# Kernel optimization log

Measured on AMD Instinct MI355X. Metric: run time of the kernel, lower is better.

Reference implementation:

```python
import jax, jax.numpy as jnp
import numpy as np
import math

D_TOKEN = 1024
N_HEADS = 16
D_HEADS = D_TOKEN // N_HEADS
B, S = 8, 4096


def setup_inputs() -> dict:
    key = jax.random.key(0)
    ks = jax.random.split(key, 8)
    scale = 1.0 / math.sqrt(D_TOKEN)
    inp = {
        "x_q": jax.random.normal(ks[0], (B, S, D_TOKEN), dtype=jnp.float32),
        "x_kv": jax.random.normal(ks[1], (B, S, D_TOKEN), dtype=jnp.float32),
        # Linear weights stored torch-style [out, in]
        "q_w": jax.random.normal(ks[2], (D_TOKEN, D_TOKEN), dtype=jnp.float32) * scale,
        "k_w": jax.random.normal(ks[3], (D_TOKEN, D_TOKEN), dtype=jnp.float32) * scale,
        "v_w": jax.random.normal(ks[4], (D_TOKEN, D_TOKEN), dtype=jnp.float32) * scale,
        "wq_w": jax.random.normal(ks[5], (N_HEADS, D_TOKEN), dtype=jnp.float32) * scale,
        "wk_w": jax.random.normal(ks[6], (N_HEADS, D_TOKEN), dtype=jnp.float32) * scale,
        "out_w": jax.random.normal(ks[7], (D_TOKEN, D_TOKEN), dtype=jnp.float32) * scale,
        # biases zero-initialized in the original module
        "q_b": jnp.zeros((D_TOKEN,), jnp.float32),
        "k_b": jnp.zeros((D_TOKEN,), jnp.float32),
        "v_b": jnp.zeros((D_TOKEN,), jnp.float32),
        "wq_b": jnp.zeros((N_HEADS,), jnp.float32),
        "wk_b": jnp.zeros((N_HEADS,), jnp.float32),
        "out_b": jnp.zeros((D_TOKEN,), jnp.float32),
    }
    return inp


def reference(x_q, x_kv, q_w, k_w, v_w, wq_w, wk_w, out_w,
              q_b, k_b, v_b, wq_b, wk_b, out_b):
    b, t, d = x_q.shape
    h, dh = N_HEADS, D_HEADS
    inv_sqrt_dh = 1.0 / math.sqrt(dh)

    q = x_q @ q_w.T + q_b          # [b, t, d]
    k = x_kv @ k_w.T + k_b         # [b, t, d]
    v = x_kv @ v_w.T + v_b         # [b, t, d]

    # query pooling: softmax over tokens (axis=1) per head
    alpha = (q @ wq_w.T + wq_b) * inv_sqrt_dh          # [b, t, h]
    alphas = jax.nn.softmax(alpha, axis=1)
    q_r = q.reshape(b, t, h, dh)
    q_global = jnp.einsum('bth,bthd->bhd', alphas, q_r).reshape(b, 1, d)

    p = k * q_global                                    # [b, t, d]

    # key pooling
    beta = (p @ wk_w.T + wk_b) * inv_sqrt_dh            # [b, t, h]
    betas = jax.nn.softmax(beta, axis=1)
    p_r = p.reshape(b, t, h, dh)
    k_global = jnp.einsum('bth,bthd->bhd', betas, p_r).reshape(b, 1, d)

    u = v * k_global                                    # [b, t, d]
    # dropout rate is 0.0 (eval/identity)
    return q + (u @ out_w.T + out_b)
```

## Files before the change

kernel.cpp:

```cpp
#include <hip/hip_runtime.h>
#include <cstdint>
#include <cstddef>

#define D_TOK 1024
#define NH 16
#define DH 64
#define BATCH 8
#define SEQ 4096
#define M_TOT (BATCH * SEQ)

typedef unsigned short u16;
typedef __attribute__((ext_vector_type(8))) __bf16 bf16x8;
typedef __attribute__((ext_vector_type(4))) float f32x4;

constexpr float INV_SQRT_DH = 0.125f;

__device__ __forceinline__ u16 f32_to_bf16_rne(float f) {
  union { float f; uint32_t u; } c; c.f = f;
  uint32_t r = (c.u + 0x7FFFu + ((c.u >> 16) & 1u)) >> 16;
  return (u16)r;
}
__device__ __forceinline__ float bf2f(u16 u) {
  union { uint32_t i; float f; } c;
  c.i = (uint32_t)u << 16;
  return c.f;
}

#define BAR() __builtin_amdgcn_s_barrier()
#define SCHB() __builtin_amdgcn_sched_barrier(0)
#define LGKM(N)                                                  \
  do {                                                           \
    asm volatile("s_waitcnt lgkmcnt(" #N ")" ::: "memory");      \
    SCHB();                                                      \
  } while (0)
#define VMW(N)                                                   \
  do {                                                           \
    asm volatile("s_waitcnt vmcnt(" #N ")" ::: "memory");        \
    SCHB();                                                      \
  } while (0)

#define GLD(GP, LP)                                               \
  __builtin_amdgcn_global_load_lds(                               \
      (const __attribute__((address_space(1))) void*)(GP),        \
      (__attribute__((address_space(3))) void*)(LP), 16, 0, 0)

template <int NN>
__global__ __launch_bounds__(256, 4) void gemm128_bf16(
    const u16* __restrict__ A, const u16* __restrict__ W0,
    const float* __restrict__ bias0, u16* __restrict__ Cb0) {
  __shared__ u16 Sh[2][2][4096];

  const int tid = threadIdx.x;
  const int lane = tid & 63;
  const int wid = tid >> 6;
  const int wr = wid >> 1;
  const int wc = wid & 1;
  const int lr = lane & 15;
  const int kg = lane >> 4;

  const int wg = blockIdx.x;
  const int cpx = gridDim.x >> 3;
  const int swz = (wg & 7) * cpx + (wg >> 3);
  const int bm0 = (swz / NN) * 128;
  const int bn0 = (swz % NN) * 128;

  f32x4 acc[4][4];
#pragma unroll
  for (int i = 0; i < 4; i++)
#pragma unroll
    for (int j = 0; j < 4; j++) acc[i][j] = (f32x4)0.f;

  const int srow = tid & 127;
  const int scg = tid >> 7;
  const u16* pA0 = A + (size_t)(bm0 + srow) * D_TOK + scg * 8;
  const u16* pB0 = W0 + (size_t)(bn0 + srow) * D_TOK + scg * 8;
  const int d0 = wid * 512;
  const int d1 = 2048 + wid * 512;
  const int aOff = (kg * 128 + wr * 64 + lr) * 16;
  const int bOff = (kg * 128 + wc * 64 + lr) * 16;

#define STG128(SL, REG)                                           \
  do {                                                            \
    const int _o = (REG) * 32;                                    \
    GLD(pA0 + _o, &Sh[SL][0][d0]);                                \
    GLD(pA0 + 16 + _o, &Sh[SL][0][d1]);                           \
    GLD(pB0 + _o, &Sh[SL][1][d0]);                                \
    GLD(pB0 + 16 + _o, &Sh[SL][1][d1]);                           \
  } while (0)

  STG128(0, 0);
  STG128(1, 1);
  VMW(4);
  BAR();

  for (int r = 0; r < 32; ++r) {
    const int sl = r & 1;
    bf16x8 af[4], bv[4];
#pragma unroll
    for (int j = 0; j < 4; ++j)
      af[j] = *reinterpret_cast<const bf16x8*>(
          (const char*)&Sh[sl][0][0] + aOff + j * 256);
#pragma unroll
    for (int n = 0; n < 4; ++n)
      bv[n] = *reinterpret_cast<const bf16x8*>(
          (const char*)&Sh[sl][1][0] + bOff + n * 256);
    LGKM(0);
    __builtin_amdgcn_s_setprio(1);
#pragma unroll
    for (int j = 0; j < 4; ++j)
#pragma unroll
      for (int n = 0; n < 4; ++n)
        acc[j][n] = __builtin_amdgcn_mfma_f32_16x16x32_bf16(
            af[j], bv[n], acc[j][n], 0, 0, 0);
    __builtin_amdgcn_s_setprio(0);
    BAR();
    if (r <= 29) {
      STG128(sl, r + 2);
      VMW(4);
      BAR();
    } else if (r == 30) {
      VMW(0);
      BAR();
    }
  }

#undef STG128

  float biasv[4];
#pragma unroll
  for (int ni = 0; ni < 4; ni++)
    biasv[ni] = bias0[bn0 + wc * 64 + ni * 16 + lr];
#pragma unroll
  for (int mi = 0; mi < 4; mi++) {
#pragma unroll
    for (int reg = 0; reg < 4; reg++) {
      const int m = bm0 + wr * 64 + mi * 16 + kg * 4 + reg;
#pragma unroll
      for (int ni = 0; ni < 4; ni++) {
        const int n = bn0 + wc * 64 + ni * 16 + lr;
        Cb0[(size_t)m * D_TOK + n] = f32_to_bf16_rne(acc[mi][ni][reg] + biasv[ni]);
      }
    }
  }
}

template <int MODE, int NN>
__global__ __launch_bounds__(512, 2) void gemm_bf16(
    const u16* __restrict__ A, const u16* __restrict__ W0,
    const float* __restrict__ bias0, const float* __restrict__ bias1,
    float* __restrict__ C, u16* __restrict__ Cb0,
    const u16* __restrict__ Rq) {
  __shared__ u16 Sh[4][2][2][4096];

  const int tid = threadIdx.x;
  const int lane = tid & 63;
  const int wid = tid >> 6;
  const int wr = wid >> 2;
  const int wc = wid & 3;
  const int wch = wc >> 1;
  const int wcl = wc & 1;
  const int lr = lane & 15;
  const int kg = lane >> 4;

  const int wg = blockIdx.x;
  const int cpx = gridDim.x >> 3;
  const int swz = (wg & 7) * cpx + (wg >> 3);
  const int bm0 = (swz / NN) * 256;
  const int bn0 = (swz % NN) * 256;
  const int b = bm0 >> 12;

  const u16* Bp = (MODE == 2) ? W0 + (size_t)b * D_TOK * D_TOK : W0;

  f32x4 acc[8][4];
#pragma unroll
  for (int i = 0; i < 8; i++)
#pragma unroll
    for (int j = 0; j < 4; j++) acc[i][j] = (f32x4)0.f;

  const int srow = tid & 127;
  const int skc = tid >> 7;
  const u16* gpA0 = A + (size_t)(bm0 + srow) * D_TOK + skc * 8;
  const u16* gpA1 = gpA0 + (size_t)128 * D_TOK;
  const u16* gpB0 = Bp + (size_t)(bn0 + srow) * D_TOK + skc * 8;
  const u16* gpB1 = gpB0 + (size_t)128 * D_TOK;
  const int widOff = wid * 512;
  const int aOff = (kg * 128 + lr) * 16;
  const int bOff = (kg * 128 + wcl * 64 + lr) * 16;

#define STAGE4(SL, REG)                                           \
  do {                                                            \
    const int _o = (REG) * 32;                                    \
    GLD(gpA0 + _o, &Sh[SL][0][0][widOff]);                        \
    GLD(gpA1 + _o, &Sh[SL][0][1][widOff]);                        \
    GLD(gpB0 + _o, &Sh[SL][1][0][widOff]);                        \
    GLD(gpB1 + _o, &Sh[SL][1][1][widOff]);                        \
  } while (0)

#define RD_A0(SL, DST)                                            \
  _Pragma("unroll") for (int j = 0; j < 4; ++j)                   \
      DST[j] = *reinterpret_cast<const bf16x8*>(                  \
          (const char*)&Sh[SL][0][wr][0] + aOff + j * 256)

#define RD_A1(SL, DST)                                            \
  _Pragma("unroll") for (int j = 0; j < 4; ++j)                   \
      DST[j] = *reinterpret_cast<const bf16x8*>(                  \
          (const char*)&Sh[SL][0][wr][0] + 1024 + aOff + j * 256)

#define RD_B(SL, DST)                                             \
  _Pragma("unroll") for (int n = 0; n < 4; ++n)                   \
      DST[n] = *reinterpret_cast<const bf16x8*>(                  \
          (const char*)&Sh[SL][1][wch][0] + bOff + n * 256)

#define MFMA_LO(BV)                                               \
  do {                                                            \
    __builtin_amdgcn_s_setprio(1);                                \
    _Pragma("unroll") for (int j = 0; j < 4; ++j)                 \
        _Pragma("unroll") for (int n = 0; n < 4; ++n)             \
            acc[j][n] = __builtin_amdgcn_mfma_f32_16x16x32_bf16(  \
                af0[j], BV[n], acc[j][n], 0, 0, 0);               \
    __builtin_amdgcn_s_setprio(0);                                \
  } while (0)

#define MFMA_HI(BV)                                               \
  do {                                                            \
    __builtin_amdgcn_s_setprio(1);                                \
    _Pragma("unroll") for (int j = 0; j < 4; ++j)                 \
        _Pragma("unroll") for (int n = 0; n < 4; ++n)             \
            acc[4 + j][n] =                                       \
                __builtin_amdgcn_mfma_f32_16x16x32_bf16(          \
                    afm[j], BV[n], acc[4 + j][n], 0, 0, 0);       \
    __builtin_amdgcn_s_setprio(0);                                \
  } while (0)

  bf16x8 af0[4], afm[4], bvE[4], bvO[4];

  STAGE4(0, 0);
  STAGE4(1, 1);
  STAGE4(2, 2);
  VMW(8);
  BAR();
  RD_A0(0, af0);
  RD_B(0, bvE);

#define UREG(SL, BVC, BVN)                                        \
  do {                                                            \
    BAR();                                                        \
    STAGE4((SL + 3) & 3, rr + 3);                                 \
    RD_A1(SL, afm);                                               \
    LGKM(4);                                                      \
    MFMA_LO(BVC);                                                 \
    VMW(8);                                                       \
    RD_A0((SL + 1) & 3, af0);                                     \
    RD_B((SL + 1) & 3, BVN);                                      \
    LGKM(8);                                                      \
    MFMA_HI(BVC);                                                 \
    ++rr;                                                         \
  } while (0)

  int rr = 0;
  for (int o = 0; o < 7; ++o) {
    UREG(0, bvE, bvO);
    UREG(1, bvO, bvE);
    UREG(2, bvE, bvO);
    UREG(3, bvO, bvE);
  }
  BAR();
  STAGE4(3, 31);
  RD_A1(0, afm);
  LGKM(4); MFMA_LO(bvE);
  VMW(8);
  RD_A0(1, af0); RD_B(1, bvO);
  LGKM(8); MFMA_HI(bvE);
  BAR();
  RD_A1(1, afm);
  LGKM(4); MFMA_LO(bvO);
  VMW(4);
  RD_A0(2, af0); RD_B(2, bvE);
  LGKM(8); MFMA_HI(bvO);
  BAR();
  RD_A1(2, afm);
  LGKM(4); MFMA_LO(bvE);
  VMW(0);
  RD_A0(3, af0); RD_B(3, bvO);
  LGKM(8); MFMA_HI(bvE);
  BAR();
  RD_A1(3, afm);
  LGKM(4); MFMA_LO(bvO);
  LGKM(0); MFMA_HI(bvO);

#undef UREG
#undef MFMA_LO
#undef MFMA_HI
#undef RD_A0
#undef RD_A1
#undef RD_B
#undef STAGE4

  float biasv[4], b1v[4];
#pragma unroll
  for (int ni = 0; ni < 4; ni++) {
    const int n = bn0 + wc * 64 + ni * 16 + lr;
    biasv[ni] = bias0[n];
    if (MODE == 2) b1v[ni] = bias1[(size_t)b * D_TOK + n];
  }
#pragma unroll
  for (int mi = 0; mi < 8; mi++) {
#pragma unroll
    for (int reg = 0; reg < 4; reg++) {
      const int m = bm0 + wr * 128 + mi * 16 + kg * 4 + reg;
#pragma unroll
      for (int ni = 0; ni < 4; ni++) {
        const int n = bn0 + wc * 64 + ni * 16 + lr;
        float o = acc[mi][ni][reg] + biasv[ni];
        if (MODE == 0) {
          Cb0[(size_t)m * D_TOK + n] = f32_to_bf16_rne(o);
        } else {
          o += b1v[ni] + bf2f(Rq[(size_t)m * D_TOK + n]);
          C[(size_t)m * D_TOK + n] = o;
        }
      }
    }
  }
}

template <int BETA>
__global__ __launch_bounds__(256) void logits_mfma(
    const u16* __restrict__ X, const float* __restrict__ W,
    const float* __restrict__ bias, const float* __restrict__ cbeta,
    float* __restrict__ alpha) {
  __shared__ u16 Wl[NH][1032];
  __shared__ u16 Xs[2][4096];

  const int tid = threadIdx.x;
  const int lane = tid & 63;
  const int wid = tid >> 6;
  const int lr = lane & 15;
  const int kg = lane >> 4;

  const int t0 = blockIdx.x * 128;
  const int b = t0 >> 12;
  const float* Wsrc = BETA ? W + (size_t)b * NH * D_TOK : W;

  for (int i = tid; i < NH * D_TOK / 4; i += 256) {
    const int r = (i * 4) >> 10, c = (i * 4) & 1023;
    const float4 v = reinterpret_cast<const float4*>(Wsrc)[i];
    ushort4 o;
    o.x = f32_to_bf16_rne(v.x);
    o.y = f32_to_bf16_rne(v.y);
    o.z = f32_to_bf16_rne(v.z);
    o.w = f32_to_bf16_rne(v.w);
    *reinterpret_cast<ushort4*>(&Wl[r][c]) = o;
  }

  const int srow = tid & 127;
  const u16* pX = X + (size_t)(t0 + srow) * D_TOK + (tid >> 7) * 8;
  const int d0 = wid * 512;
  const int d1 = 2048 + wid * 512;
  const int aOff = (kg * 128 + wid * 32 + lr) * 16;

#define STGL(SL, REG)                                             \
  do {                                                            \
    const int _o = (REG) * 32;                                    \
    GLD(pX + _o, &Xs[SL][d0]);                                    \
    GLD(pX + 16 + _o, &Xs[SL][d1]);                               \
  } while (0)

  STGL(0, 0);
  STGL(1, 1);
  __syncthreads();

  f32x4 acc[2];
  acc[0] = (f32x4)0.f;
  acc[1] = (f32x4)0.f;

  for (int r = 0; r < 32; ++r) {
    const int sl = r & 1;
    bf16x8 af[2], bv;
#pragma unroll
    for (int j = 0; j < 2; ++j)
      af[j] = *reinterpret_cast<const bf16x8*>(
          (const char*)&Xs[sl][0] + aOff + j * 256);
    bv = *reinterpret_cast<const bf16x8*>(
        (const char*)&Wl[lr][0] + r * 64 + kg * 16);
    LGKM(0);
#pragma unroll
    for (int j = 0; j < 2; ++j)
      acc[j] = __builtin_amdgcn_mfma_f32_16x16x32_bf16(af[j], bv, acc[j], 0, 0, 0);
    BAR();
    if (r <= 29) {
      STGL(sl, r + 2);
      VMW(2);
      BAR();
    } else if (r == 30) {
      VMW(0);
      BAR();
    }
  }

#undef STGL

  const float bv_ = bias[lr] + (BETA ? cbeta[b * NH + lr] : 0.f);
#pragma unroll
  for (int j = 0; j < 2; ++j) {
#pragma unroll
    for (int reg = 0; reg < 4; ++reg) {
      const int t = t0 + wid * 32 + j * 16 + kg * 4 + reg;
      alpha[(size_t)t * NH + lr] = (acc[j][reg] + bv_) * INV_SQRT_DH;
    }
  }
}

__global__ __launch_bounds__(256) void cvt_all(
    const float* __restrict__ a, const float* __restrict__ bsrc,
    const float* __restrict__ qw, u16* __restrict__ oa,
    u16* __restrict__ ob, u16* __restrict__ oqw) {
  const int half = M_TOT * D_TOK / 4;
  const int wq4 = D_TOK * D_TOK / 4;
  int i = blockIdx.x * 256 + threadIdx.x;
  const int stride = gridDim.x * 256;
  for (; i < 2 * half + wq4; i += stride) {
    const float* src;
    u16* dst;
    int j;
    if (i < half) { src = a; dst = oa; j = i; }
    else if (i < 2 * half) { src = bsrc; dst = ob; j = i - half; }
    else { src = qw; dst = oqw; j = i - 2 * half; }
    const float4 v = reinterpret_cast<const float4*>(src)[j];
    ushort4 o;
    o.x = f32_to_bf16_rne(v.x);
    o.y = f32_to_bf16_rne(v.y);
    o.z = f32_to_bf16_rne(v.z);
    o.w = f32_to_bf16_rne(v.w);
    reinterpret_cast<ushort4*>(dst)[j] = o;
  }
}

__global__ __launch_bounds__(256) void transpose_vw(
    const float* __restrict__ v_w, u16* __restrict__ vwT) {
  __shared__ float tile[64][65];
  const int r0 = (blockIdx.x >> 4) * 64;
  const int c0 = (blockIdx.x & 15) * 64;
  for (int i = threadIdx.x; i < 4096; i += 256) {
    const int r = i >> 6, c = i & 63;
    tile[r][c] = v_w[(size_t)(r0 + r) * D_TOK + c0 + c];
  }
  __syncthreads();
  for (int i = threadIdx.x; i < 4096; i += 256) {
    const int rr = i >> 6, cc = i & 63;
    vwT[(size_t)(c0 + rr) * D_TOK + r0 + cc] = f32_to_bf16_rne(tile[cc][rr]);
  }
}

__global__ __launch_bounds__(256) void scale_vbt(
    const float* __restrict__ ow, const float* __restrict__ kglb,
    const float* __restrict__ v_b, u16* __restrict__ owsc,
    float* __restrict__ vbt) {
  const int per_b = D_TOK * D_TOK / 4;
  int i = blockIdx.x * 256 + threadIdx.x;
  const int stride = gridDim.x * 256;
  const int lane = threadIdx.x & 63;
  for (; i < BATCH * per_b; i += stride) {
    const int b = i >> 18, j = i & (per_b - 1);
    const int k4 = j & 255, n = j >> 8;
    const float4 w = reinterpret_cast<const float4*>(ow)[j];
    const float4 s = reinterpret_cast<const float4*>(kglb)[b * 256 + k4];
    const float4 v = reinterpret_cast<const float4*>(v_b)[k4];
    const float wsx = w.x * s.x, wsy = w.y * s.y, wsz = w.z * s.z,
                wsw = w.w * s.w;
    ushort4 o;
    o.x = f32_to_bf16_rne(wsx);
    o.y = f32_to_bf16_rne(wsy);
    o.z = f32_to_bf16_rne(wsz);
    o.w = f32_to_bf16_rne(wsw);
    reinterpret_cast<ushort4*>(owsc)[i] = o;
    float p = wsx * v.x + wsy * v.y + wsz * v.z + wsw * v.w;
#pragma unroll
    for (int off = 32; off; off >>= 1) p += __shfl_xor(p, off, 64);
    if (lane == 0) atomicAdd(&vbt[(size_t)b * D_TOK + n], p);
  }
}

__global__ __launch_bounds__(256) void mb2_kernel(
    const float* __restrict__ k_w, const float* __restrict__ wk,
    const float* __restrict__ qg, const float* __restrict__ k_b,
    float* __restrict__ Mb, float* __restrict__ cbeta) {
  __shared__ float wq[128 * 16];
  const int bidx = blockIdx.x;
  const int b = bidx >> 5;
  const int nc = (bidx >> 3) & 3;
  const int dc = bidx & 7;
  const int n = nc * 256 + threadIdx.x;
  const int d0 = dc * 128;
  const int tid = threadIdx.x;

  for (int e = tid; e < 128 * 16; e += 256) {
    const int d = e >> 4, h = e & 15;
    wq[e] = qg[(size_t)b * D_TOK + d0 + d] * wk[(size_t)h * D_TOK + d0 + d];
  }
  __syncthreads();

  float acc[NH];
#pragma unroll
  for (int h = 0; h < NH; h++) acc[h] = 0.f;
#pragma unroll 4
  for (int d = 0; d < 128; ++d) {
    const float kv = k_w[(size_t)(d0 + d) * D_TOK + n];
#pragma unroll
    for (int h = 0; h < NH; h++) acc[h] += kv * wq[d * 16 + h];
  }
#pragma unroll
  for (int h = 0; h < NH; h++)
    atomicAdd(&Mb[((size_t)b * NH + h) * D_TOK + n], acc[h]);

  if (nc == 0 && tid < 64) {
    const int h = tid & 15, dl = tid >> 4;
    float c = 0.f;
    for (int d = dl; d < 128; d += 4)
      c += k_b[d0 + d] * wq[d * 16 + h];
    c += __shfl_xor(c, 16, 64);
    c += __shfl_xor(c, 32, 64);
    if (dl == 0) atomicAdd(&cbeta[b * NH + h], c);
  }
}

__global__ __launch_bounds__(256) void kglb2_kernel(
    const float* __restrict__ xp, const float* __restrict__ k_w,
    const float* __restrict__ qg, const float* __restrict__ k_b,
    float* __restrict__ kglb) {
  __shared__ float xs[D_TOK];
  const int b = blockIdx.x >> 6;
  const int d0 = (blockIdx.x & 63) * 16;
  const int h = d0 >> 6;
  const int tid = threadIdx.x, lane = tid & 63, wv = tid >> 6;

  reinterpret_cast<float4*>(xs)[tid] =
      reinterpret_cast<const float4*>(xp + ((size_t)b * NH + h) * D_TOK)[tid];
  __syncthreads();

#pragma unroll
  for (int i = 0; i < 4; ++i) {
    const int d = d0 + wv * 4 + i;
    const float4* kr = reinterpret_cast<const float4*>(k_w + (size_t)d * D_TOK);
    float s = 0.f;
#pragma unroll
    for (int k4 = 0; k4 < 4; ++k4) {
      const int j4 = lane + k4 * 64;
      const float4 kv = kr[j4];
      const float4 xv = reinterpret_cast<const float4*>(xs)[j4];
      s += kv.x * xv.x + kv.y * xv.y + kv.z * xv.z + kv.w * xv.w;
    }
#pragma unroll
    for (int off = 32; off; off >>= 1) s += __shfl_xor(s, off, 64);
    if (lane == 0)
      kglb[(size_t)b * D_TOK + d] = qg[(size_t)b * D_TOK + d] * (s + k_b[d]);
  }
}

__global__ __launch_bounds__(256) void softmax_prep(
    const float* __restrict__ al, float* __restrict__ smx,
    float* __restrict__ sinv) {
  __shared__ float red[4];
  const int b = blockIdx.x >> 4, h = blockIdx.x & 15;
  const int tid = threadIdx.x, lane = tid & 63, wid = tid >> 6;
  const float* col = al + (size_t)b * SEQ * NH + h;

  float mx = -INFINITY;
  for (int t = tid; t < SEQ; t += 256) mx = fmaxf(mx, col[(size_t)t * NH]);
#pragma unroll
  for (int off = 32; off; off >>= 1) mx = fmaxf(mx, __shfl_xor(mx, off, 64));
  if (lane == 0) red[wid] = mx;
  __syncthreads();
  mx = fmaxf(fmaxf(red[0], red[1]), fmaxf(red[2], red[3]));
  __syncthreads();

  float s = 0.f;
  for (int t = tid; t < SEQ; t += 256) s += __expf(col[(size_t)t * NH] - mx);
#pragma unroll
  for (int off = 32; off; off >>= 1) s += __shfl_xor(s, off, 64);
  if (lane == 0) red[wid] = s;
  __syncthreads();
  if (tid == 0) {
    const float tot = red[0] + red[1] + red[2] + red[3];
    smx[blockIdx.x] = mx;
    sinv[blockIdx.x] = 1.0f / tot;
  }
}

__global__ __launch_bounds__(256) void pool_accum_bf(
    const float* __restrict__ al, const u16* __restrict__ src,
    const float* __restrict__ smx, const float* __restrict__ sinv,
    float* __restrict__ g) {
  constexpr int TCH = 64;
  const int b = blockIdx.x / (SEQ / TCH);
  const int t0 = (blockIdx.x % (SEQ / TCH)) * TCH;
  const int d0 = threadIdx.x * 4;
  const int h = d0 >> 6;
  const float mx = smx[b * NH + h];
  const float inv = sinv[b * NH + h];

  float4 acc = make_float4(0.f, 0.f, 0.f, 0.f);
  const float* ap = al + ((size_t)b * SEQ + t0) * NH + h;
  const u16* sp = src + ((size_t)b * SEQ + t0) * D_TOK + d0;
#pragma unroll 2
  for (int t = 0; t < TCH; t++) {
    const float wgt = __expf(ap[(size_t)t * NH] - mx) * inv;
    const ushort4 v = *reinterpret_cast<const ushort4*>(sp + (size_t)t * D_TOK);
    acc.x += wgt * bf2f(v.x);
    acc.y += wgt * bf2f(v.y);
    acc.z += wgt * bf2f(v.z);
    acc.w += wgt * bf2f(v.w);
  }
  float* gp = g + (size_t)b * D_TOK + d0;
  atomicAdd(gp + 0, acc.x);
  atomicAdd(gp + 1, acc.y);
  atomicAdd(gp + 2, acc.z);
  atomicAdd(gp + 3, acc.w);
}

__global__ __launch_bounds__(256) void xp_pool(
    const float* __restrict__ al, const u16* __restrict__ x,
    const float* __restrict__ smx, const float* __restrict__ sinv,
    float* __restrict__ xp) {
  constexpr int TCH = 128;
  __shared__ float wl[TCH][NH];
  const int b = blockIdx.x >> 5;
  const int t0 = (blockIdx.x & 31) * TCH;
  const int tid = threadIdx.x;
  for (int i = tid; i < TCH * NH; i += 256) {
    const int tt = i >> 4, h = i & 15;
    wl[tt][h] = __expf(al[((size_t)(b * SEQ + t0 + tt)) * NH + h] -
                       smx[b * NH + h]) *
                sinv[b * NH + h];
  }
  __syncthreads();

  const int n0 = tid * 4;
  float acc[NH][4];
#pragma unroll
  for (int h = 0; h < NH; h++)
#pragma unroll
    for (int c = 0; c < 4; c++) acc[h][c] = 0.f;
  const u16* xpt = x + ((size_t)b * SEQ + t0) * D_TOK + n0;
  for (int tt = 0; tt < TCH; tt++) {
    const ushort4 v = *reinterpret_cast<const ushort4*>(xpt + (size_t)tt * D_TOK);
    const float x0 = bf2f(v.x), x1 = bf2f(v.y), x2 = bf2f(v.z), x3 = bf2f(v.w);
#pragma unroll
    for (int h = 0; h < NH; h++) {
      const float w = wl[tt][h];
      acc[h][0] += w * x0;
      acc[h][1] += w * x1;
      acc[h][2] += w * x2;
      acc[h][3] += w * x3;
    }
  }
#pragma unroll
  for (int h = 0; h < NH; h++)
#pragma unroll
    for (int c = 0; c < 4; c++)
      atomicAdd(&xp[((size_t)b * NH + h) * D_TOK + n0 + c], acc[h][c]);
}

extern "C" void kernel_launch(void* const* d_in, const int* in_sizes, int n_in,
                              void* d_out, int out_size, void* d_ws,
                              size_t ws_size, hipStream_t stream) {
  const float* x_q   = (const float*)d_in[0];
  const float* x_kv  = (const float*)d_in[1];
  const float* q_w   = (const float*)d_in[2];
  const float* k_w   = (const float*)d_in[3];
  const float* v_w   = (const float*)d_in[4];
  const float* wq_w  = (const float*)d_in[5];
  const float* wk_w  = (const float*)d_in[6];
  const float* out_w = (const float*)d_in[7];
  const float* q_b   = (const float*)d_in[8];
  const float* k_b   = (const float*)d_in[9];
  const float* v_b   = (const float*)d_in[10];
  const float* wq_b  = (const float*)d_in[11];
  const float* wk_b  = (const float*)d_in[12];
  const float* out_b = (const float*)d_in[13];
  float* out = (float*)d_out;

  char* ws = (char*)d_ws;
  const size_t SZ_BF  = (size_t)M_TOT * D_TOK * sizeof(u16);
  const size_t SZ_WBF = (size_t)D_TOK * D_TOK * sizeof(u16);
  size_t off = 0;
  u16* xq_bf  = (u16*)(ws + off); off += SZ_BF;
  u16* xkv_bf = (u16*)(ws + off); off += SZ_BF;
  u16* q_bf   = (u16*)(ws + off); off += SZ_BF;
  u16* qw_bf  = (u16*)(ws + off); off += SZ_WBF;
  u16* vwT_bf = (u16*)(ws + off); off += SZ_WBF;
  u16* owsc   = (u16*)(ws + off); off += BATCH * SZ_WBF;
  u16* Nbt    = (u16*)(ws + off); off += BATCH * SZ_WBF;
  float* Mb   = (float*)(ws + off); off += (size_t)BATCH * NH * D_TOK * 4;
  float* xp   = (float*)(ws + off); off += (size_t)BATCH * NH * D_TOK * 4;
  float* al   = (float*)(ws + off); off += (size_t)M_TOT * NH * 4;
  float* qg   = (float*)(ws + off); off += BATCH * D_TOK * 4;
  float* kglb = (float*)(ws + off); off += BATCH * D_TOK * 4;
  float* vbt  = (float*)(ws + off); off += BATCH * D_TOK * 4;
  float* zb   = (float*)(ws + off); off += D_TOK * 4;
  float* cbeta= (float*)(ws + off); off += BATCH * NH * 4;
  float* smx0 = (float*)(ws + off); off += BATCH * NH * 4;
  float* sinv0= (float*)(ws + off); off += BATCH * NH * 4;
  float* smx1 = (float*)(ws + off); off += BATCH * NH * 4;
  float* sinv1= (float*)(ws + off); off += BATCH * NH * 4;

  hipMemsetAsync(qg, 0, BATCH * D_TOK * 4, stream);
  hipMemsetAsync(xp, 0, (size_t)BATCH * NH * D_TOK * 4, stream);
  hipMemsetAsync(zb, 0, D_TOK * 4, stream);
  hipMemsetAsync(Mb, 0, (size_t)BATCH * NH * D_TOK * 4, stream);
  hipMemsetAsync(cbeta, 0, BATCH * NH * 4, stream);
  hipMemsetAsync(vbt, 0, BATCH * D_TOK * 4, stream);

  cvt_all<<<2048, 256, 0, stream>>>(x_q, x_kv, q_w, xq_bf, xkv_bf, qw_bf);
  transpose_vw<<<256, 256, 0, stream>>>(v_w, vwT_bf);

  gemm_bf16<0, 4><<<512, 512, 0, stream>>>(xq_bf, qw_bf, q_b, nullptr,
                                           nullptr, q_bf, nullptr);
  logits_mfma<0><<<256, 256, 0, stream>>>(q_bf, wq_w, wq_b, nullptr, al);
  softmax_prep<<<BATCH * NH, 256, 0, stream>>>(al, smx0, sinv0);
  pool_accum_bf<<<BATCH * (SEQ / 64), 256, 0, stream>>>(al, q_bf, smx0, sinv0,
                                                        qg);
  mb2_kernel<<<256, 256, 0, stream>>>(k_w, wk_w, qg, k_b, Mb, cbeta);
  logits_mfma<1><<<256, 256, 0, stream>>>(xkv_bf, Mb, wk_b, cbeta, al);
  softmax_prep<<<BATCH * NH, 256, 0, stream>>>(al, smx1, sinv1);
  xp_pool<<<256, 256, 0, stream>>>(al, xkv_bf, smx1, sinv1, xp);
  kglb2_kernel<<<512, 256, 0, stream>>>(xp, k_w, qg, k_b, kglb);
  scale_vbt<<<1024, 256, 0, stream>>>(out_w, kglb, v_b, owsc, vbt);
  gemm128_bf16<8><<<512, 256, 0, stream>>>(owsc, vwT_bf, zb, Nbt);
  gemm_bf16<2, 4><<<512, 512, 0, stream>>>(xkv_bf, Nbt, out_b, vbt, out,
                                           nullptr, q_bf);
}
```

Before: 565.6 us.

## Merge conversion kernels, coalesce memsets, simplify gemm128 and logits pipelines

```diff
diff --git a/kernel.cpp b/kernel.cpp
--- a/kernel.cpp
+++ b/kernel.cpp
@@ -45,7 +45,7 @@
       (__attribute__((address_space(3))) void*)(LP), 16, 0, 0)
 
 template <int NN>
-__global__ __launch_bounds__(256, 4) void gemm128_bf16(
+__global__ __launch_bounds__(256) void gemm128_bf16(
     const u16* __restrict__ A, const u16* __restrict__ W0,
     const float* __restrict__ bias0, u16* __restrict__ Cb0) {
   __shared__ u16 Sh[2][2][4096];
@@ -89,12 +89,11 @@
   } while (0)
 
   STG128(0, 0);
-  STG128(1, 1);
-  VMW(4);
-  BAR();
+  __syncthreads();
 
   for (int r = 0; r < 32; ++r) {
     const int sl = r & 1;
+    if (r < 31) STG128(sl ^ 1, r + 1);
     bf16x8 af[4], bv[4];
 #pragma unroll
     for (int j = 0; j < 4; ++j)
@@ -104,24 +103,13 @@
     for (int n = 0; n < 4; ++n)
       bv[n] = *reinterpret_cast<const bf16x8*>(
           (const char*)&Sh[sl][1][0] + bOff + n * 256);
-    LGKM(0);
-    __builtin_amdgcn_s_setprio(1);
 #pragma unroll
     for (int j = 0; j < 4; ++j)
 #pragma unroll
       for (int n = 0; n < 4; ++n)
         acc[j][n] = __builtin_amdgcn_mfma_f32_16x16x32_bf16(
             af[j], bv[n], acc[j][n], 0, 0, 0);
-    __builtin_amdgcn_s_setprio(0);
-    BAR();
-    if (r <= 29) {
-      STG128(sl, r + 2);
-      VMW(4);
-      BAR();
-    } else if (r == 30) {
-      VMW(0);
-      BAR();
-    }
+    __syncthreads();
   }
 
 #undef STG128
@@ -366,7 +354,6 @@
   } while (0)
 
   STGL(0, 0);
-  STGL(1, 1);
   __syncthreads();
 
   f32x4 acc[2];
@@ -375,6 +362,7 @@
 
   for (int r = 0; r < 32; ++r) {
     const int sl = r & 1;
+    if (r < 31) STGL(sl ^ 1, r + 1);
     bf16x8 af[2], bv;
 #pragma unroll
     for (int j = 0; j < 2; ++j)
@@ -382,19 +370,10 @@
           (const char*)&Xs[sl][0] + aOff + j * 256);
     bv = *reinterpret_cast<const bf16x8*>(
         (const char*)&Wl[lr][0] + r * 64 + kg * 16);
-    LGKM(0);
 #pragma unroll
     for (int j = 0; j < 2; ++j)
       acc[j] = __builtin_amdgcn_mfma_f32_16x16x32_bf16(af[j], bv, acc[j], 0, 0, 0);
-    BAR();
-    if (r <= 29) {
-      STGL(sl, r + 2);
-      VMW(2);
-      BAR();
-    } else if (r == 30) {
-      VMW(0);
-      BAR();
-    }
+    __syncthreads();
   }
 
 #undef STGL
@@ -412,42 +391,43 @@
 
 __global__ __launch_bounds__(256) void cvt_all(
     const float* __restrict__ a, const float* __restrict__ bsrc,
-    const float* __restrict__ qw, u16* __restrict__ oa,
-    u16* __restrict__ ob, u16* __restrict__ oqw) {
-  const int half = M_TOT * D_TOK / 4;
-  const int wq4 = D_TOK * D_TOK / 4;
-  int i = blockIdx.x * 256 + threadIdx.x;
-  const int stride = gridDim.x * 256;
-  for (; i < 2 * half + wq4; i += stride) {
-    const float* src;
-    u16* dst;
-    int j;
-    if (i < half) { src = a; dst = oa; j = i; }
-    else if (i < 2 * half) { src = bsrc; dst = ob; j = i - half; }
-    else { src = qw; dst = oqw; j = i - 2 * half; }
-    const float4 v = reinterpret_cast<const float4*>(src)[j];
-    ushort4 o;
-    o.x = f32_to_bf16_rne(v.x);
-    o.y = f32_to_bf16_rne(v.y);
-    o.z = f32_to_bf16_rne(v.z);
-    o.w = f32_to_bf16_rne(v.w);
-    reinterpret_cast<ushort4*>(dst)[j] = o;
-  }
-}
-
-__global__ __launch_bounds__(256) void transpose_vw(
-    const float* __restrict__ v_w, u16* __restrict__ vwT) {
+    const float* __restrict__ qw, const float* __restrict__ v_w,
+    u16* __restrict__ oa, u16* __restrict__ ob, u16* __restrict__ oqw,
+    u16* __restrict__ vwT) {
   __shared__ float tile[64][65];
-  const int r0 = (blockIdx.x >> 4) * 64;
-  const int c0 = (blockIdx.x & 15) * 64;
-  for (int i = threadIdx.x; i < 4096; i += 256) {
-    const int r = i >> 6, c = i & 63;
-    tile[r][c] = v_w[(size_t)(r0 + r) * D_TOK + c0 + c];
-  }
-  __syncthreads();
-  for (int i = threadIdx.x; i < 4096; i += 256) {
-    const int rr = i >> 6, cc = i & 63;
-    vwT[(size_t)(c0 + rr) * D_TOK + r0 + cc] = f32_to_bf16_rne(tile[cc][rr]);
+  if (blockIdx.x < 2048) {
+    const int half = M_TOT * D_TOK / 4;
+    const int wq4 = D_TOK * D_TOK / 4;
+    int i = blockIdx.x * 256 + threadIdx.x;
+    const int stride = 2048 * 256;
+    for (; i < 2 * half + wq4; i += stride) {
+      const float* src;
+      u16* dst;
+      int j;
+      if (i < half) { src = a; dst = oa; j = i; }
+      else if (i < 2 * half) { src = bsrc; dst = ob; j = i - half; }
+      else { src = qw; dst = oqw; j = i - 2 * half; }
+      const float4 v = reinterpret_cast<const float4*>(src)[j];
+      ushort4 o;
+      o.x = f32_to_bf16_rne(v.x);
+      o.y = f32_to_bf16_rne(v.y);
+      o.z = f32_to_bf16_rne(v.z);
+      o.w = f32_to_bf16_rne(v.w);
+      reinterpret_cast<ushort4*>(dst)[j] = o;
+    }
+  } else {
+    const int tb = blockIdx.x - 2048;
+    const int r0 = (tb >> 4) * 64;
+    const int c0 = (tb & 15) * 64;
+    for (int i = threadIdx.x; i < 4096; i += 256) {
+      const int r = i >> 6, c = i & 63;
+      tile[r][c] = v_w[(size_t)(r0 + r) * D_TOK + c0 + c];
+    }
+    __syncthreads();
+    for (int i = threadIdx.x; i < 4096; i += 256) {
+      const int rr = i >> 6, cc = i & 63;
+      vwT[(size_t)(c0 + rr) * D_TOK + r0 + cc] = f32_to_bf16_rne(tile[cc][rr]);
+    }
   }
 }
 
@@ -690,28 +670,25 @@
   u16* vwT_bf = (u16*)(ws + off); off += SZ_WBF;
   u16* owsc   = (u16*)(ws + off); off += BATCH * SZ_WBF;
   u16* Nbt    = (u16*)(ws + off); off += BATCH * SZ_WBF;
-  float* Mb   = (float*)(ws + off); off += (size_t)BATCH * NH * D_TOK * 4;
-  float* xp   = (float*)(ws + off); off += (size_t)BATCH * NH * D_TOK * 4;
   float* al   = (float*)(ws + off); off += (size_t)M_TOT * NH * 4;
-  float* qg   = (float*)(ws + off); off += BATCH * D_TOK * 4;
   float* kglb = (float*)(ws + off); off += BATCH * D_TOK * 4;
-  float* vbt  = (float*)(ws + off); off += BATCH * D_TOK * 4;
-  float* zb   = (float*)(ws + off); off += D_TOK * 4;
-  float* cbeta= (float*)(ws + off); off += BATCH * NH * 4;
   float* smx0 = (float*)(ws + off); off += BATCH * NH * 4;
   float* sinv0= (float*)(ws + off); off += BATCH * NH * 4;
   float* smx1 = (float*)(ws + off); off += BATCH * NH * 4;
   float* sinv1= (float*)(ws + off); off += BATCH * NH * 4;
-
-  hipMemsetAsync(qg, 0, BATCH * D_TOK * 4, stream);
-  hipMemsetAsync(xp, 0, (size_t)BATCH * NH * D_TOK * 4, stream);
-  hipMemsetAsync(zb, 0, D_TOK * 4, stream);
-  hipMemsetAsync(Mb, 0, (size_t)BATCH * NH * D_TOK * 4, stream);
-  hipMemsetAsync(cbeta, 0, BATCH * NH * 4, stream);
-  hipMemsetAsync(vbt, 0, BATCH * D_TOK * 4, stream);
-
-  cvt_all<<<2048, 256, 0, stream>>>(x_q, x_kv, q_w, xq_bf, xkv_bf, qw_bf);
-  transpose_vw<<<256, 256, 0, stream>>>(v_w, vwT_bf);
+  char* zstart = ws + off;
+  float* xp   = (float*)(ws + off); off += (size_t)BATCH * NH * D_TOK * 4;
+  float* Mb   = (float*)(ws + off); off += (size_t)BATCH * NH * D_TOK * 4;
+  float* qg   = (float*)(ws + off); off += BATCH * D_TOK * 4;
+  float* vbt  = (float*)(ws + off); off += BATCH * D_TOK * 4;
+  float* zb   = (float*)(ws + off); off += D_TOK * 4;
+  float* cbeta= (float*)(ws + off); off += BATCH * NH * 4;
+  const size_t ZTOT = (size_t)(ws + off - zstart);
+
+  hipMemsetAsync(zstart, 0, ZTOT, stream);
+
+  cvt_all<<<2304, 256, 0, stream>>>(x_q, x_kv, q_w, v_w, xq_bf, xkv_bf,
+                                    qw_bf, vwT_bf);
 
   gemm_bf16<0, 4><<<512, 512, 0, stream>>>(xq_bf, qw_bf, q_b, nullptr,
                                            nullptr, q_bf, nullptr);
```

Result: faster. 552.3 us (-2.4%).
